# Kernel tuning notes

Hardware: AMD Instinct MI355X
Metric: run time of the kernel (lower is better)

Reference implementation:

```python
import jax, jax.numpy as jnp
import numpy as np

N, E, G, H, NI, EI, OUT, L = 100000, 800000, 256, 96, 32, 10, 256, 3


def setup_inputs() -> dict:
    key = jax.random.key(0)
    ks = jax.random.split(key, 32)
    s = 0.05  # small weight scale to keep activations finite over 3 layers
    d = {}
    d['x'] = jax.random.normal(ks[0], (N, NI), dtype=jnp.float32)
    d['edge_attr'] = jax.random.normal(ks[1], (E, EI), dtype=jnp.float32)
    d['edge_index'] = jax.random.randint(ks[2], (2, E), 0, N)
    d['batch_idx'] = jnp.sort(jax.random.randint(ks[3], (N,), 0, G))
    d['node_W'] = jax.random.normal(ks[4], (NI, H)) * s
    d['node_b'] = jnp.zeros((H,))
    d['edge_W'] = jax.random.normal(ks[5], (EI, H)) * s
    d['edge_b'] = jnp.zeros((H,))
    d['mlp_W1'] = jax.random.normal(ks[6], (L, H, H)) * s
    d['mlp_b1'] = jnp.zeros((L, H))
    d['mlp_W2'] = jax.random.normal(ks[7], (L, H, H)) * s
    d['mlp_b2'] = jnp.zeros((L, H))
    d['eps'] = jnp.zeros((L,))            # GINEConv train_eps, init 0
    d['gn_w'] = jnp.ones((L, H))          # GraphNorm weight
    d['gn_b'] = jnp.zeros((L, H))         # GraphNorm bias
    d['gn_ms'] = jnp.ones((L, H))         # GraphNorm mean_scale
    d['ln_g'] = jnp.ones((2 * H,))        # LayerNorm gamma
    d['ln_b'] = jnp.zeros((2 * H,))       # LayerNorm beta
    d['out_W1'] = jax.random.normal(ks[8], (2 * H, H)) * s
    d['out_b1'] = jnp.zeros((H,))
    d['out_W2'] = jax.random.normal(ks[9], (H, OUT)) * s
    d['out_b2'] = jnp.zeros((OUT,))
    return d


def reference(x, edge_attr, edge_index, batch_idx, node_W, node_b, edge_W, edge_b,
              mlp_W1, mlp_b1, mlp_W2, mlp_b2, eps, gn_w, gn_b, gn_ms,
              ln_g, ln_b, out_W1, out_b1, out_W2, out_b2):
    n = x.shape[0]
    src, dst = edge_index[0], edge_index[1]
    h = jax.nn.relu(x @ node_W + node_b)            # [N, H]
    e = jax.nn.relu(edge_attr @ edge_W + edge_b)    # [E, H]
    cnt = jax.ops.segment_sum(jnp.ones((n, 1), h.dtype), batch_idx, num_segments=G)
    cnt = jnp.maximum(cnt, 1.0)
    for i in range(L):
        res = h
        # GINEConv: msg = relu(x_src + e), sum-aggregate at dst
        msg = jax.nn.relu(h[src] + e)
        agg = jax.ops.segment_sum(msg, dst, num_segments=n)
        z = (1.0 + eps[i]) * h + agg
        z = jax.nn.relu(z @ mlp_W1[i] + mlp_b1[i]) @ mlp_W2[i] + mlp_b2[i]
        # GraphNorm (per-graph, per-feature)
        mean = jax.ops.segment_sum(z, batch_idx, num_segments=G) / cnt
        out = z - mean[batch_idx] * gn_ms[i]
        var = jax.ops.segment_sum(out * out, batch_idx, num_segments=G) / cnt
        z = gn_w[i] * out / jnp.sqrt(var + 1e-5)[batch_idx] + gn_b[i]
        h = jax.nn.relu(z) + res  # dropout is identity in eval
    gmean = jax.ops.segment_sum(h, batch_idx, num_segments=G) / cnt
    gmax = jax.ops.segment_max(h, batch_idx, num_segments=G)
    g = jnp.concatenate([gmean, gmax], axis=1)       # [G, 2H]
    mu = g.mean(axis=-1, keepdims=True)
    va = jnp.mean((g - mu) ** 2, axis=-1, keepdims=True)
    g = (g - mu) / jnp.sqrt(va + 1e-5) * ln_g + ln_b
    return jax.nn.relu(g @ out_W1 + out_b1) @ out_W2 + out_b2
```

## Files before the change

### kernel.cpp

```cpp
#include <hip/hip_runtime.h>
#include <hip/hip_bf16.h>
#include <cfloat>

#define Nn 100000
#define Ee 800000
#define Gg 256
#define NBLK ((Nn + 255) / 256)

typedef __attribute__((ext_vector_type(8))) short short8;
typedef __attribute__((ext_vector_type(4))) float f32x4;
typedef unsigned short u16;

static __device__ __forceinline__ float blo(unsigned u) { return __builtin_bit_cast(float, u << 16); }
static __device__ __forceinline__ float bhi(unsigned u) { return __builtin_bit_cast(float, u & 0xffff0000u); }
static __device__ __forceinline__ float bus(u16 u) { return __builtin_bit_cast(float, ((unsigned)u) << 16); }
static __device__ __forceinline__ u16 f2bu(float f) {
  __hip_bfloat16 b = __float2bfloat16(f);
  return __builtin_bit_cast(u16, b);
}
static __device__ __forceinline__ unsigned pack2(float lo, float hi) {
  return (unsigned)f2bu(lo) | ((unsigned)f2bu(hi) << 16);
}


__global__ __launch_bounds__(512) void k_gptr(const int* __restrict__ batch, int* __restrict__ gptr) {
  int g = threadIdx.x;
  if (g > Gg) return;
  if (g == Gg) { gptr[Gg] = Nn; return; }
  int lo = 0, hi = Nn;
  while (lo < hi) { int mid = (lo + hi) >> 1; if (batch[mid] < g) lo = mid + 1; else hi = mid; }
  gptr[g] = lo;
}

__global__ __launch_bounds__(256) void k_deg(const int* __restrict__ dst, int* __restrict__ deg) {
  int e = blockIdx.x * 256 + threadIdx.x;
  if (e < Ee) atomicAdd(&deg[dst[e]], 1);
}

__global__ __launch_bounds__(256) void k_scanA(const int* __restrict__ deg, int* __restrict__ localA,
                                               int* __restrict__ bsum) {
  __shared__ int ts[256];
  int t = threadIdx.x, b = blockIdx.x;
  int base = b * 1024 + t * 4;
  int v[4]; int s = 0;
#pragma unroll
  for (int k = 0; k < 4; k++) { int idx = base + k; v[k] = (idx < Nn) ? deg[idx] : 0; s += v[k]; }
  ts[t] = s; __syncthreads();
  for (int off = 1; off < 256; off <<= 1) {
    int y = (t >= off) ? ts[t - off] : 0;
    __syncthreads();
    ts[t] += y;
    __syncthreads();
  }
  int ex = ts[t] - s;
#pragma unroll
  for (int k = 0; k < 4; k++) { int idx = base + k; if (idx < Nn) localA[idx] = ex; ex += v[k]; }
  if (t == 255) bsum[b] = ts[255];
}

__global__ __launch_bounds__(128) void k_scanB(int* __restrict__ bsum) {
  __shared__ int s[128];
  const int NB = (Nn + 1023) / 1024;
  int t = threadIdx.x;
  int v = (t < NB) ? bsum[t] : 0;
  s[t] = v; __syncthreads();
  for (int off = 1; off < 128; off <<= 1) {
    int y = (t >= off) ? s[t - off] : 0;
    __syncthreads();
    s[t] += y;
    __syncthreads();
  }
  if (t < NB) bsum[t] = s[t] - v;
}

__global__ __launch_bounds__(256) void k_scanC(const int* __restrict__ localA, const int* __restrict__ bsum,
                                               int* __restrict__ rowptr, int* __restrict__ cursor) {
  int i = blockIdx.x * 256 + threadIdx.x;
  if (i < Nn) { int v = localA[i] + bsum[i >> 10]; rowptr[i] = v; cursor[i] = v; }
  if (i == 0) rowptr[Nn] = Ee;
}

__global__ __launch_bounds__(256) void k_fill(const int* __restrict__ dst, int* __restrict__ cursor,
                                              int* __restrict__ elist) {
  int e = blockIdx.x * 256 + threadIdx.x;
  if (e < Ee) { int p = atomicAdd(&cursor[dst[e]], 1); elist[p] = e; }
}


__global__ __launch_bounds__(256) void k_dhistA(const int* __restrict__ deg, int* __restrict__ bhist) {
  __shared__ int lh[64];
  int t = threadIdx.x, blk = blockIdx.x;
  if (t < 64) lh[t] = 0;
  __syncthreads();
  int i = blk * 256 + t;
  if (i < Nn) atomicAdd(&lh[min(deg[i], 63)], 1);
  __syncthreads();
  if (t < 64) bhist[blk * 64 + t] = lh[t];
}

__global__ void k_dscanB(int* __restrict__ bhist, int* __restrict__ binbase) {
  int bin = threadIdx.x;
  int running = 0;
  for (int blk = 0; blk < NBLK; blk++) {
    int v = bhist[blk * 64 + bin];
    bhist[blk * 64 + bin] = running;
    running += v;
  }
  int tot = running;
  int x = tot;
#pragma unroll
  for (int off = 1; off < 64; off <<= 1) {
    int y = __shfl_up(x, off);
    if (bin >= off) x += y;
  }
  binbase[bin] = x - tot;
}

__global__ __launch_bounds__(256) void k_dfillC(const int* __restrict__ deg, const int* __restrict__ bhist,
                                                const int* __restrict__ binbase, int* __restrict__ nperm) {
  __shared__ int lh[64];
  int t = threadIdx.x, blk = blockIdx.x;
  if (t < 64) lh[t] = 0;
  __syncthreads();
  int i = blk * 256 + t;
  if (i < Nn) {
    int bin = min(deg[i], 63);
    int lrank = atomicAdd(&lh[bin], 1);
    nperm[binbase[bin] + bhist[blk * 64 + bin] + lrank] = i;
  }
}


#define EB 128

__global__ __launch_bounds__(192) void k_edge_mlp(const float* __restrict__ eattr, const int* __restrict__ elist,
                                                  const int* __restrict__ srcArr, const float* __restrict__ eW,
                                                  const float* __restrict__ eb, u16* __restrict__ ePerm,
                                                  int* __restrict__ srcPerm) {
  __shared__ float ea[EB][10];
  __shared__ float Ws[10 * 96];
  __shared__ float bs[96];
  int t = threadIdx.x;
  int q0 = blockIdx.x * EB;
  int m = min(EB, Ee - q0);
  for (int i = t; i < 960; i += 192) Ws[i] = eW[i];
  if (t < 96) bs[t] = eb[t];
  for (int i = t; i < m; i += 192) srcPerm[q0 + i] = srcArr[elist[q0 + i]];
  for (int i = t; i < 5 * m; i += 192) {
    int ii = i / 5, k2 = (i - ii * 5) * 2;
    int e = elist[q0 + ii];
    *reinterpret_cast<float2*>(&ea[ii][k2]) = *reinterpret_cast<const float2*>(&eattr[(size_t)e * 10 + k2]);
  }
  __syncthreads();
  int j = (t % 48) * 2, sub = t / 48;
  float b0 = bs[j], b1 = bs[j + 1];
  for (int i = sub; i < m; i += 4) {
    float acc0 = b0, acc1 = b1;
#pragma unroll
    for (int k = 0; k < 10; k++) {
      float a = ea[i][k];
      float2 w = *reinterpret_cast<const float2*>(&Ws[k * 96 + j]);
      acc0 += a * w.x; acc1 += a * w.y;
    }
    *reinterpret_cast<unsigned*>(ePerm + (size_t)(q0 + i) * 96 + j) =
        pack2(fmaxf(acc0, 0.f), fmaxf(acc1, 0.f));
  }
}


__global__ __launch_bounds__(256) void k_node_mlp(const float* __restrict__ x, const float* __restrict__ W,
                                                  const float* __restrict__ b, u16* __restrict__ h16) {
  __shared__ float xs[16][33];
  __shared__ float Ws[32 * 96];
  __shared__ float bs[96];
  int t = threadIdx.x;
  int n0 = blockIdx.x * 16;
  for (int i = t; i < 32 * 96; i += 256) Ws[i] = W[i];
  if (t < 96) bs[t] = b[t];
  for (int i = t; i < 512; i += 256) {
    int nl = i >> 5, k = i & 31; int n = n0 + nl;
    xs[nl][k] = (n < Nn) ? x[n * 32 + k] : 0.f;
  }
  __syncthreads();
#pragma unroll
  for (int p = 0; p < 6; p++) {
    int oi = t + p * 256; int nl = oi / 96, j = oi % 96; int n = n0 + nl;
    if (n < Nn) {
      float acc = bs[j];
#pragma unroll
      for (int k = 0; k < 32; k++) acc += xs[nl][k] * Ws[k * 96 + j];
      h16[(size_t)n * 96 + j] = f2bu(fmaxf(acc, 0.f));
    }
  }
}


#define MPAD 104

#define ACC8(hv, ev, B) \
  acc[B+0] += fmaxf(blo(hv.x) + blo(ev.x), 0.f); acc[B+1] += fmaxf(bhi(hv.x) + bhi(ev.x), 0.f); \
  acc[B+2] += fmaxf(blo(hv.y) + blo(ev.y), 0.f); acc[B+3] += fmaxf(bhi(hv.y) + bhi(ev.y), 0.f); \
  acc[B+4] += fmaxf(blo(hv.z) + blo(ev.z), 0.f); acc[B+5] += fmaxf(bhi(hv.z) + bhi(ev.z), 0.f); \
  acc[B+6] += fmaxf(blo(hv.w) + blo(ev.w), 0.f); acc[B+7] += fmaxf(bhi(hv.w) + bhi(ev.w), 0.f);

#define LOAD6(hp, ep, H0, H1, H2, E0, E1, E2) \
  uint4 H0 = *reinterpret_cast<const uint4*>(hp); \
  uint4 H1 = *reinterpret_cast<const uint4*>(hp + 8); \
  uint4 H2 = *reinterpret_cast<const uint4*>(hp + 16); \
  uint4 E0 = *reinterpret_cast<const uint4*>(ep); \
  uint4 E1 = *reinterpret_cast<const uint4*>(ep + 8); \
  uint4 E2 = *reinterpret_cast<const uint4*>(ep + 16);

__global__ __launch_bounds__(256) void k_layer(const u16* __restrict__ h16,
                                               const u16* __restrict__ ePerm,
                                               const int* __restrict__ srcPerm,
                                               const int* __restrict__ rowptr,
                                               const int* __restrict__ nperm,
                                               const float* __restrict__ W1, const float* __restrict__ b1,
                                               const float* __restrict__ W2, const float* __restrict__ b2,
                                               const float* __restrict__ epsA, int layer,
                                               float* __restrict__ z) {
  __shared__ __align__(16) __hip_bfloat16 At[64][MPAD];
  __shared__ __align__(16) __hip_bfloat16 Wt[96][MPAD];
  __shared__ int snode[64], sbeg[64], send[64];
  int t = threadIdx.x;
  int n0 = blockIdx.x * 64;
  if (t < 64) {
    int idx = n0 + t;
    int node = (idx < Nn) ? nperm[idx] : -1;
    snode[t] = node;
    sbeg[t] = (node >= 0) ? rowptr[node] : 0;
    send[t] = (node >= 0) ? rowptr[node + 1] : 0;
  }
  __syncthreads();
  float epsv = 1.0f + epsA[layer];
  int nl = t >> 2, q = t & 3;
  int beg = sbeg[nl], end = send[nl];
  int node = snode[nl];
  const size_t fo = (size_t)q * 24;
  float acc[24];
#pragma unroll
  for (int j = 0; j < 24; j++) acc[j] = 0.f;
  int e = beg;
  for (; e + 3 <= end; e += 3) {
    int s0 = srcPerm[e], s1 = srcPerm[e + 1], s2 = srcPerm[e + 2];
    const u16* hp0 = h16 + (size_t)s0 * 96 + fo;
    const u16* hp1 = h16 + (size_t)s1 * 96 + fo;
    const u16* hp2 = h16 + (size_t)s2 * 96 + fo;
    const u16* ep0 = ePerm + (size_t)e * 96 + fo;
    const u16* ep1 = ePerm + (size_t)(e + 1) * 96 + fo;
    const u16* ep2 = ePerm + (size_t)(e + 2) * 96 + fo;
    LOAD6(hp0, ep0, ha0, ha1, ha2, ea0, ea1, ea2)
    LOAD6(hp1, ep1, hb0, hb1, hb2, eb0, eb1, eb2)
    LOAD6(hp2, ep2, hc0, hc1, hc2, ec0, ec1, ec2)
    ACC8(ha0, ea0, 0)
    ACC8(ha1, ea1, 8)
    ACC8(ha2, ea2, 16)
    ACC8(hb0, eb0, 0)
    ACC8(hb1, eb1, 8)
    ACC8(hb2, eb2, 16)
    ACC8(hc0, ec0, 0)
    ACC8(hc1, ec1, 8)
    ACC8(hc2, ec2, 16)
  }
  for (; e < end; e++) {
    int s0 = srcPerm[e];
    const u16* hp0 = h16 + (size_t)s0 * 96 + fo;
    const u16* ep0 = ePerm + (size_t)e * 96 + fo;
    LOAD6(hp0, ep0, ha0, ha1, ha2, ea0, ea1, ea2)
    ACC8(ha0, ea0, 0)
    ACC8(ha1, ea1, 8)
    ACC8(ha2, ea2, 16)
  }
  {
    uint4 hh0 = make_uint4(0, 0, 0, 0), hh1 = hh0, hh2 = hh0;
    if (node >= 0) {
      const u16* hp = h16 + (size_t)node * 96 + fo;
      hh0 = *reinterpret_cast<const uint4*>(hp);
      hh1 = *reinterpret_cast<const uint4*>(hp + 8);
      hh2 = *reinterpret_cast<const uint4*>(hp + 16);
    }
    uint4 w0, w1, w2;
    w0.x = pack2(fmaf(epsv, blo(hh0.x), acc[0]),  fmaf(epsv, bhi(hh0.x), acc[1]));
    w0.y = pack2(fmaf(epsv, blo(hh0.y), acc[2]),  fmaf(epsv, bhi(hh0.y), acc[3]));
    w0.z = pack2(fmaf(epsv, blo(hh0.z), acc[4]),  fmaf(epsv, bhi(hh0.z), acc[5]));
    w0.w = pack2(fmaf(epsv, blo(hh0.w), acc[6]),  fmaf(epsv, bhi(hh0.w), acc[7]));
    w1.x = pack2(fmaf(epsv, blo(hh1.x), acc[8]),  fmaf(epsv, bhi(hh1.x), acc[9]));
    w1.y = pack2(fmaf(epsv, blo(hh1.y), acc[10]), fmaf(epsv, bhi(hh1.y), acc[11]));
    w1.z = pack2(fmaf(epsv, blo(hh1.z), acc[12]), fmaf(epsv, bhi(hh1.z), acc[13]));
    w1.w = pack2(fmaf(epsv, blo(hh1.w), acc[14]), fmaf(epsv, bhi(hh1.w), acc[15]));
    w2.x = pack2(fmaf(epsv, blo(hh2.x), acc[16]), fmaf(epsv, bhi(hh2.x), acc[17]));
    w2.y = pack2(fmaf(epsv, blo(hh2.y), acc[18]), fmaf(epsv, bhi(hh2.y), acc[19]));
    w2.z = pack2(fmaf(epsv, blo(hh2.z), acc[20]), fmaf(epsv, bhi(hh2.z), acc[21]));
    w2.w = pack2(fmaf(epsv, blo(hh2.w), acc[22]), fmaf(epsv, bhi(hh2.w), acc[23]));
    *reinterpret_cast<uint4*>(&At[nl][fo]) = w0;
    *reinterpret_cast<uint4*>(&At[nl][fo + 8]) = w1;
    *reinterpret_cast<uint4*>(&At[nl][fo + 16]) = w2;
  }
  for (int i = t; i < 24 * 96; i += 256) {
    int kg = i / 96, c = i - kg * 96;
    int k0 = kg * 4;
    float w0 = W1[(k0 + 0) * 96 + c];
    float w1 = W1[(k0 + 1) * 96 + c];
    float w2 = W1[(k0 + 2) * 96 + c];
    float w3 = W1[(k0 + 3) * 96 + c];
    *reinterpret_cast<uint2*>(&Wt[c][k0]) = make_uint2(pack2(w0, w1), pack2(w2, w3));
  }
  __syncthreads();
  int w = t >> 6, l = t & 63;
  int lr = l & 15, lg = l >> 4;
  int rowBase = w * 16;
  short8 a0 = *reinterpret_cast<const short8*>(&At[rowBase + lr][lg * 8]);
  short8 a1 = *reinterpret_cast<const short8*>(&At[rowBase + lr][32 + lg * 8]);
  short8 a2 = *reinterpret_cast<const short8*>(&At[rowBase + lr][64 + lg * 8]);
  f32x4 gacc[6];
#pragma unroll
  for (int nt = 0; nt < 6; nt++) gacc[nt] = (f32x4){0.f, 0.f, 0.f, 0.f};
#pragma unroll
  for (int nt = 0; nt < 6; nt++) {
    short8 b0 = *reinterpret_cast<const short8*>(&Wt[nt * 16 + lr][lg * 8]);
    short8 bv1 = *reinterpret_cast<const short8*>(&Wt[nt * 16 + lr][32 + lg * 8]);
    short8 bv2 = *reinterpret_cast<const short8*>(&Wt[nt * 16 + lr][64 + lg * 8]);
    gacc[nt] = __builtin_amdgcn_mfma_f32_16x16x32_bf16(a0, b0, gacc[nt], 0, 0, 0);
    gacc[nt] = __builtin_amdgcn_mfma_f32_16x16x32_bf16(a1, bv1, gacc[nt], 0, 0, 0);
    gacc[nt] = __builtin_amdgcn_mfma_f32_16x16x32_bf16(a2, bv2, gacc[nt], 0, 0, 0);
  }
#pragma unroll
  for (int nt = 0; nt < 6; nt++) {
    int col = nt * 16 + lr;
    float bias = b1[col];
#pragma unroll
    for (int j = 0; j < 4; j++) {
      int row = rowBase + lg * 4 + j;
      At[row][col] = __float2bfloat16(fmaxf(gacc[nt][j] + bias, 0.f));
    }
  }
  __syncthreads();
  for (int i = t; i < 24 * 96; i += 256) {
    int kg = i / 96, c = i - kg * 96;
    int k0 = kg * 4;
    float w0 = W2[(k0 + 0) * 96 + c];
    float w1 = W2[(k0 + 1) * 96 + c];
    float w2 = W2[(k0 + 2) * 96 + c];
    float w3 = W2[(k0 + 3) * 96 + c];
    *reinterpret_cast<uint2*>(&Wt[c][k0]) = make_uint2(pack2(w0, w1), pack2(w2, w3));
  }
  __syncthreads();
  short8 m0 = *reinterpret_cast<const short8*>(&At[rowBase + lr][lg * 8]);
  short8 m1 = *reinterpret_cast<const short8*>(&At[rowBase + lr][32 + lg * 8]);
  short8 m2 = *reinterpret_cast<const short8*>(&At[rowBase + lr][64 + lg * 8]);
#pragma unroll
  for (int nt = 0; nt < 6; nt++) gacc[nt] = (f32x4){0.f, 0.f, 0.f, 0.f};
#pragma unroll
  for (int nt = 0; nt < 6; nt++) {
    short8 b0 = *reinterpret_cast<const short8*>(&Wt[nt * 16 + lr][lg * 8]);
    short8 bv1 = *reinterpret_cast<const short8*>(&Wt[nt * 16 + lr][32 + lg * 8]);
    short8 bv2 = *reinterpret_cast<const short8*>(&Wt[nt * 16 + lr][64 + lg * 8]);
    gacc[nt] = __builtin_amdgcn_mfma_f32_16x16x32_bf16(m0, b0, gacc[nt], 0, 0, 0);
    gacc[nt] = __builtin_amdgcn_mfma_f32_16x16x32_bf16(m1, bv1, gacc[nt], 0, 0, 0);
    gacc[nt] = __builtin_amdgcn_mfma_f32_16x16x32_bf16(m2, bv2, gacc[nt], 0, 0, 0);
  }
#pragma unroll
  for (int nt = 0; nt < 6; nt++) {
    int col = nt * 16 + lr;
    float bias = b2[col];
#pragma unroll
    for (int j = 0; j < 4; j++) {
      int row = rowBase + lg * 4 + j;
      int n = snode[row];
      if (n >= 0) z[(size_t)n * 96 + col] = gacc[nt][j] + bias;
    }
  }
}


#define ACHUNK 32

__global__ __launch_bounds__(128) void k_agg(const u16* __restrict__ h16, const float* __restrict__ eattr,
                                             const int* __restrict__ srcArr, const int* __restrict__ rowptr,
                                             const int* __restrict__ elist, const float* __restrict__ eW,
                                             const float* __restrict__ eb, float* __restrict__ agg) {
  __shared__ float Ws[10 * 96];
  __shared__ float bs_s[96];
  __shared__ int sL[ACHUNK];
  __shared__ float eaL[ACHUNK][10];
  int t = threadIdx.x;
  int nd = blockIdx.x;
  for (int i = t; i < 960; i += 128) Ws[i] = eW[i];
  if (t < 96) bs_s[t] = eb[t];
  int beg = rowptr[nd], end = rowptr[nd + 1];
  float acc = 0.f;
  for (int cs = beg; cs < end; cs += ACHUNK) {
    int m = min(ACHUNK, end - cs);
    __syncthreads();
    if (t < m) sL[t] = srcArr[elist[cs + t]];
    for (int i = t; i < 10 * m; i += 128) {
      int ii = i / 10, k = i - ii * 10;
      int e = elist[cs + ii];
      eaL[ii][k] = eattr[(size_t)e * 10 + k];
    }
    __syncthreads();
    if (t < 96) {
#pragma unroll 4
      for (int i = 0; i < m; i++) {
        int src = sL[i];
        float ej = bs_s[t];
#pragma unroll
        for (int k = 0; k < 10; k++) ej += eaL[i][k] * Ws[k * 96 + t];
        ej = fmaxf(ej, 0.f);
        acc += fmaxf(bus(h16[(size_t)src * 96 + t]) + ej, 0.f);
      }
    }
  }
  if (t < 96) agg[(size_t)nd * 96 + t] = acc;
}


__global__ __launch_bounds__(256) void k_mlp_fb(const u16* __restrict__ h16, const float* agg,
                                                const float* __restrict__ W1, const float* __restrict__ b1,
                                                const float* __restrict__ W2, const float* __restrict__ b2,
                                                const float* __restrict__ epsA, int layer, float* z) {
  __shared__ __align__(16) __hip_bfloat16 At[64][MPAD];
  __shared__ __align__(16) __hip_bfloat16 Wt[96][MPAD];
  __shared__ __align__(16) __hip_bfloat16 md[64][MPAD];
  int t = threadIdx.x;
  int n0 = blockIdx.x * 64;
  float epsv = 1.0f + epsA[layer];
  for (int i = t; i < 64 * 24; i += 256) {
    int r = i / 24, sl = (i - r * 24) * 4;
    int n = n0 + r;
    unsigned plo = 0, phi = 0;
    if (n < Nn) {
      uint2 hv = *reinterpret_cast<const uint2*>(h16 + (size_t)n * 96 + sl);
      float4 av = *reinterpret_cast<const float4*>(agg + (size_t)n * 96 + sl);
      plo = pack2(epsv * blo(hv.x) + av.x, epsv * bhi(hv.x) + av.y);
      phi = pack2(epsv * blo(hv.y) + av.z, epsv * bhi(hv.y) + av.w);
    }
    *reinterpret_cast<uint2*>(&At[r][sl]) = make_uint2(plo, phi);
  }
  for (int i = t; i < 24 * 96; i += 256) {
    int kg = i / 96, c = i - kg * 96;
    int k0 = kg * 4;
    float w0 = W1[(k0 + 0) * 96 + c];
    float w1 = W1[(k0 + 1) * 96 + c];
    float w2 = W1[(k0 + 2) * 96 + c];
    float w3 = W1[(k0 + 3) * 96 + c];
    *reinterpret_cast<uint2*>(&Wt[c][k0]) = make_uint2(pack2(w0, w1), pack2(w2, w3));
  }
  __syncthreads();
  int w = t >> 6, l = t & 63;
  int lr = l & 15, lg = l >> 4;
  int rowBase = w * 16;
  short8 a0 = *reinterpret_cast<const short8*>(&At[rowBase + lr][lg * 8]);
  short8 a1 = *reinterpret_cast<const short8*>(&At[rowBase + lr][32 + lg * 8]);
  short8 a2 = *reinterpret_cast<const short8*>(&At[rowBase + lr][64 + lg * 8]);
  f32x4 acc[6];
#pragma unroll
  for (int nt = 0; nt < 6; nt++) acc[nt] = (f32x4){0.f, 0.f, 0.f, 0.f};
#pragma unroll
  for (int nt = 0; nt < 6; nt++) {
    short8 b0 = *reinterpret_cast<const short8*>(&Wt[nt * 16 + lr][lg * 8]);
    short8 bv1 = *reinterpret_cast<const short8*>(&Wt[nt * 16 + lr][32 + lg * 8]);
    short8 bv2 = *reinterpret_cast<const short8*>(&Wt[nt * 16 + lr][64 + lg * 8]);
    acc[nt] = __builtin_amdgcn_mfma_f32_16x16x32_bf16(a0, b0, acc[nt], 0, 0, 0);
    acc[nt] = __builtin_amdgcn_mfma_f32_16x16x32_bf16(a1, bv1, acc[nt], 0, 0, 0);
    acc[nt] = __builtin_amdgcn_mfma_f32_16x16x32_bf16(a2, bv2, acc[nt], 0, 0, 0);
  }
#pragma unroll
  for (int nt = 0; nt < 6; nt++) {
    int col = nt * 16 + lr;
    float bias = b1[col];
#pragma unroll
    for (int j = 0; j < 4; j++) {
      int row = rowBase + lg * 4 + j;
      md[row][col] = __float2bfloat16(fmaxf(acc[nt][j] + bias, 0.f));
    }
  }
  __syncthreads();
  for (int i = t; i < 24 * 96; i += 256) {
    int kg = i / 96, c = i - kg * 96;
    int k0 = kg * 4;
    float w0 = W2[(k0 + 0) * 96 + c];
    float w1 = W2[(k0 + 1) * 96 + c];
    float w2 = W2[(k0 + 2) * 96 + c];
    float w3 = W2[(k0 + 3) * 96 + c];
    *reinterpret_cast<uint2*>(&Wt[c][k0]) = make_uint2(pack2(w0, w1), pack2(w2, w3));
  }
  __syncthreads();
  short8 m0 = *reinterpret_cast<const short8*>(&md[rowBase + lr][lg * 8]);
  short8 m1 = *reinterpret_cast<const short8*>(&md[rowBase + lr][32 + lg * 8]);
  short8 m2 = *reinterpret_cast<const short8*>(&md[rowBase + lr][64 + lg * 8]);
#pragma unroll
  for (int nt = 0; nt < 6; nt++) acc[nt] = (f32x4){0.f, 0.f, 0.f, 0.f};
#pragma unroll
  for (int nt = 0; nt < 6; nt++) {
    short8 b0 = *reinterpret_cast<const short8*>(&Wt[nt * 16 + lr][lg * 8]);
    short8 bv1 = *reinterpret_cast<const short8*>(&Wt[nt * 16 + lr][32 + lg * 8]);
    short8 bv2 = *reinterpret_cast<const short8*>(&Wt[nt * 16 + lr][64 + lg * 8]);
    acc[nt] = __builtin_amdgcn_mfma_f32_16x16x32_bf16(m0, b0, acc[nt], 0, 0, 0);
    acc[nt] = __builtin_amdgcn_mfma_f32_16x16x32_bf16(m1, bv1, acc[nt], 0, 0, 0);
    acc[nt] = __builtin_amdgcn_mfma_f32_16x16x32_bf16(m2, bv2, acc[nt], 0, 0, 0);
  }
#pragma unroll
  for (int nt = 0; nt < 6; nt++) {
    int col = nt * 16 + lr;
    float bias = b2[col];
#pragma unroll
    for (int j = 0; j < 4; j++) {
      int row = rowBase + lg * 4 + j;
      int n = n0 + row;
      if (n < Nn) z[(size_t)n * 96 + col] = acc[nt][j] + bias;
    }
  }
}


__global__ __launch_bounds__(384) void k_gnorm(const float* __restrict__ z, u16* __restrict__ h16,
                                               const int* __restrict__ gptr, const float* __restrict__ ms,
                                               const float* __restrict__ gw, const float* __restrict__ gb) {
  __shared__ float r1[16][100];
  __shared__ float r2[16][100];
  __shared__ float smm[96], sinv[96], sgb[96];
  int g = blockIdx.x, t = threadIdx.x;
  int beg = gptr[g], end = gptr[g + 1];
  int sub = t / 24, slot = t - (t / 24) * 24;
  int sl = slot * 4;
  float4 s1 = make_float4(0.f, 0.f, 0.f, 0.f), s2 = s1;
  for (int n = beg + sub; n < end; n += 16) {
    float4 zv = *reinterpret_cast<const float4*>(z + (size_t)n * 96 + sl);
    s1.x += zv.x; s1.y += zv.y; s1.z += zv.z; s1.w += zv.w;
    s2.x += zv.x * zv.x; s2.y += zv.y * zv.y; s2.z += zv.z * zv.z; s2.w += zv.w * zv.w;
  }
  *reinterpret_cast<float4*>(&r1[sub][sl]) = s1;
  *reinterpret_cast<float4*>(&r2[sub][sl]) = s2;
  __syncthreads();
  if (t < 96) {
    float S1 = 0.f, S2 = 0.f;
#pragma unroll
    for (int u = 0; u < 16; u++) { S1 += r1[u][t]; S2 += r2[u][t]; }
    float c = (float)max(end - beg, 1);
    float m = S1 / c;
    float mm = m * ms[t];
    float var = S2 / c - 2.f * mm * m + mm * mm;
    var = fmaxf(var, 0.f);
    smm[t] = mm;
    sinv[t] = rsqrtf(var + 1e-5f) * gw[t];
    sgb[t] = gb[t];
  }
  __syncthreads();
  float4 mm4 = *reinterpret_cast<const float4*>(&smm[sl]);
  float4 iv4 = *reinterpret_cast<const float4*>(&sinv[sl]);
  float4 gb4 = *reinterpret_cast<const float4*>(&sgb[sl]);
  for (int n = beg + sub; n < end; n += 16) {
    float4 zv = *reinterpret_cast<const float4*>(z + (size_t)n * 96 + sl);
    uint2 hv = *reinterpret_cast<const uint2*>(h16 + (size_t)n * 96 + sl);
    float o0 = fmaxf((zv.x - mm4.x) * iv4.x + gb4.x, 0.f) + blo(hv.x);
    float o1 = fmaxf((zv.y - mm4.y) * iv4.y + gb4.y, 0.f) + bhi(hv.x);
    float o2 = fmaxf((zv.z - mm4.z) * iv4.z + gb4.z, 0.f) + blo(hv.y);
    float o3 = fmaxf((zv.w - mm4.w) * iv4.w + gb4.w, 0.f) + bhi(hv.y);
    *reinterpret_cast<uint2*>(h16 + (size_t)n * 96 + sl) = make_uint2(pack2(o0, o1), pack2(o2, o3));
  }
}


__global__ __launch_bounds__(256) void k_pool_out(const u16* __restrict__ h16, const int* __restrict__ gptr,
                                                  const float* __restrict__ lng, const float* __restrict__ lnb,
                                                  const float* __restrict__ W1, const float* __restrict__ b1,
                                                  const float* __restrict__ W2, const float* __restrict__ b2,
                                                  float* __restrict__ out) {
  __shared__ float sh1[2][96], sh2[2][96];
  __shared__ float gbuf[192];
  __shared__ float rs[4], rq[4];
  __shared__ float s_mu, s_rstd;
  __shared__ float inter[96];
  int g = blockIdx.x, t = threadIdx.x;
  int beg = gptr[g], end = gptr[g + 1];
  if (t < 192) {
    int j = t % 96, half = t / 96;
    float s = 0.f, m = -INFINITY;
    for (int n = beg + half; n < end; n += 2) {
      float v = bus(h16[(size_t)n * 96 + j]);
      s += v; m = fmaxf(m, v);
    }
    sh1[half][j] = s; sh2[half][j] = m;
  }
  __syncthreads();
  if (t < 96) {
    float c = (float)max(end - beg, 1);
    gbuf[t] = (sh1[0][t] + sh1[1][t]) / c;
    gbuf[96 + t] = fmaxf(sh2[0][t], sh2[1][t]);
  }
  __syncthreads();
  float sv = (t < 192) ? gbuf[t] : 0.f;
  float qv = sv * sv;
#pragma unroll
  for (int off = 32; off; off >>= 1) { sv += __shfl_down(sv, off); qv += __shfl_down(qv, off); }
  if ((t & 63) == 0) { rs[t >> 6] = sv; rq[t >> 6] = qv; }
  __syncthreads();
  if (t == 0) {
    float S = rs[0] + rs[1] + rs[2] + rs[3];
    float Q = rq[0] + rq[1] + rq[2] + rq[3];
    float mu = S / 192.f;
    float va = Q / 192.f - mu * mu;
    s_mu = mu; s_rstd = rsqrtf(fmaxf(va, 0.f) + 1e-5f);
  }
  __syncthreads();
  if (t < 192) gbuf[t] = (gbuf[t] - s_mu) * s_rstd * lng[t] + lnb[t];
  __syncthreads();
  if (t < 96) {
    float a = b1[t];
    for (int k = 0; k < 192; k++) a += gbuf[k] * W1[k * 96 + t];
    inter[t] = fmaxf(a, 0.f);
  }
  __syncthreads();
  {
    float a = b2[t];
    for (int j = 0; j < 96; j++) a += inter[j] * W2[j * 256 + t];
    out[g * 256 + t] = a;
  }
}


extern "C" void kernel_launch(void* const* d_in, const int* in_sizes, int n_in,
                              void* d_out, int out_size, void* d_ws, size_t ws_size,
                              hipStream_t stream) {
  (void)in_sizes; (void)n_in; (void)out_size;
  const float* x     = (const float*)d_in[0];
  const float* eattr = (const float*)d_in[1];
  const int*   eidx2 = (const int*)  d_in[2];
  const int*   batch = (const int*)  d_in[3];
  const float* nodeW = (const float*)d_in[4];
  const float* nodeb = (const float*)d_in[5];
  const float* edgeW = (const float*)d_in[6];
  const float* edgeb = (const float*)d_in[7];
  const float* mlpW1 = (const float*)d_in[8];
  const float* mlpb1 = (const float*)d_in[9];
  const float* mlpW2 = (const float*)d_in[10];
  const float* mlpb2 = (const float*)d_in[11];
  const float* epsA  = (const float*)d_in[12];
  const float* gnw   = (const float*)d_in[13];
  const float* gnb   = (const float*)d_in[14];
  const float* gnms  = (const float*)d_in[15];
  const float* lng   = (const float*)d_in[16];
  const float* lnb   = (const float*)d_in[17];
  const float* oW1   = (const float*)d_in[18];
  const float* ob1   = (const float*)d_in[19];
  const float* oW2   = (const float*)d_in[20];
  const float* ob2   = (const float*)d_in[21];
  float* out = (float*)d_out;

  const int* srcArr = eidx2;
  const int* dstArr = eidx2 + Ee;

  char* p = (char*)d_ws;
  auto carve = [&](size_t bytes) -> void* {
    void* r = (void*)p;
    p += ((bytes + 255) & ~(size_t)255);
    return r;
  };
  u16* h16     = (u16*)carve((size_t)Nn * 96 * 2);
  float* aggz  = (float*)carve((size_t)Nn * 96 * 4);
  int* rowptr  = (int*)carve((size_t)(Nn + 1) * 4);
  int* elist   = (int*)carve((size_t)Ee * 4);
  int* gptr    = (int*)carve((size_t)(Gg + 1) * 4);
  int* nperm   = (int*)carve((size_t)Nn * 4);
  int* bhist   = (int*)carve((size_t)NBLK * 64 * 4);
  int* binbase = (int*)carve(64 * 4);
  int* srcPerm = (int*)carve((size_t)Ee * 4);
  int* deg     = srcPerm;
  int* localA  = srcPerm + Nn;
  int* cursor  = srcPerm + 2 * Nn;
  int* bsum    = srcPerm + 3 * Nn;
  u16* ePerm = (u16*)carve((size_t)Ee * 96 * 2);
  bool pre = ((size_t)(p - (char*)d_ws)) <= ws_size;

  hipMemsetAsync(deg, 0, (size_t)Nn * 4, stream);
  k_gptr<<<1, 512, 0, stream>>>(batch, gptr);
  k_deg<<<(Ee + 255) / 256, 256, 0, stream>>>(dstArr, deg);
  k_scanA<<<(Nn + 1023) / 1024, 256, 0, stream>>>(deg, localA, bsum);
  k_scanB<<<1, 128, 0, stream>>>(bsum);
  k_scanC<<<(Nn + 255) / 256, 256, 0, stream>>>(localA, bsum, rowptr, cursor);
  k_fill<<<(Ee + 255) / 256, 256, 0, stream>>>(dstArr, cursor, elist);

  if (pre) {
    k_dhistA<<<NBLK, 256, 0, stream>>>(deg, bhist);
    k_dscanB<<<1, 64, 0, stream>>>(bhist, binbase);
    k_dfillC<<<NBLK, 256, 0, stream>>>(deg, bhist, binbase, nperm);
    k_edge_mlp<<<(Ee + EB - 1) / EB, 192, 0, stream>>>(eattr, elist, srcArr, edgeW, edgeb, ePerm, srcPerm);
  }

  k_node_mlp<<<(Nn + 15) / 16, 256, 0, stream>>>(x, nodeW, nodeb, h16);

  for (int i = 0; i < 3; i++) {
    if (pre) {
      k_layer<<<(Nn + 63) / 64, 256, 0, stream>>>(h16, ePerm, srcPerm, rowptr, nperm,
                                                  mlpW1 + i * 9216, mlpb1 + i * 96,
                                                  mlpW2 + i * 9216, mlpb2 + i * 96, epsA, i, aggz);
    } else {
      k_agg<<<Nn, 128, 0, stream>>>(h16, eattr, srcArr, rowptr, elist, edgeW, edgeb, aggz);
      k_mlp_fb<<<(Nn + 63) / 64, 256, 0, stream>>>(h16, aggz, mlpW1 + i * 9216, mlpb1 + i * 96,
                                                   mlpW2 + i * 9216, mlpb2 + i * 96, epsA, i, aggz);
    }
    k_gnorm<<<Gg, 384, 0, stream>>>(aggz, h16, gptr, gnms + i * 96, gnw + i * 96, gnb + i * 96);
  }

  k_pool_out<<<Gg, 256, 0, stream>>>(h16, gptr, lng, lnb, oW1, ob1, oW2, ob2, out);
}
```

Measured before the change: 591.4 us.

## Build CSR in degree-sorted node order so layer edges are contiguous per block

The CSR row pointers and the edge list are now built in the degree-sorted node permutation order. A rank array maps each original node to its sorted position, and the scan and fill run over that order. Each layer block's edges then form one contiguous range, so the ePerm and srcPerm reads are sequential across the block and rowptr loads become a single coalesced 65-entry read. The cost is an extra rank kernel and indirect gathers in the scan and fill, and the fallback path keeps the original CSR.

```diff
diff --git a/kernel.cpp b/kernel.cpp
--- a/kernel.cpp
+++ b/kernel.cpp
@@ -45,6 +45,27 @@
   int v[4]; int s = 0;
 #pragma unroll
   for (int k = 0; k < 4; k++) { int idx = base + k; v[k] = (idx < Nn) ? deg[idx] : 0; s += v[k]; }
+  ts[t] = s; __syncthreads();
+  for (int off = 1; off < 256; off <<= 1) {
+    int y = (t >= off) ? ts[t - off] : 0;
+    __syncthreads();
+    ts[t] += y;
+    __syncthreads();
+  }
+  int ex = ts[t] - s;
+#pragma unroll
+  for (int k = 0; k < 4; k++) { int idx = base + k; if (idx < Nn) localA[idx] = ex; ex += v[k]; }
+  if (t == 255) bsum[b] = ts[255];
+}
+
+__global__ __launch_bounds__(256) void k_scanA2(const int* __restrict__ deg, const int* __restrict__ nperm,
+                                                int* __restrict__ localA, int* __restrict__ bsum) {
+  __shared__ int ts[256];
+  int t = threadIdx.x, b = blockIdx.x;
+  int base = b * 1024 + t * 4;
+  int v[4]; int s = 0;
+#pragma unroll
+  for (int k = 0; k < 4; k++) { int idx = base + k; v[k] = (idx < Nn) ? deg[nperm[idx]] : 0; s += v[k]; }
   ts[t] = s; __syncthreads();
   for (int off = 1; off < 256; off <<= 1) {
     int y = (t >= off) ? ts[t - off] : 0;
@@ -86,6 +107,12 @@
   if (e < Ee) { int p = atomicAdd(&cursor[dst[e]], 1); elist[p] = e; }
 }
 
+__global__ __launch_bounds__(256) void k_fill2(const int* __restrict__ dst, const int* __restrict__ rank,
+                                               int* __restrict__ cursor, int* __restrict__ elist) {
+  int e = blockIdx.x * 256 + threadIdx.x;
+  if (e < Ee) { int p = atomicAdd(&cursor[rank[dst[e]]], 1); elist[p] = e; }
+}
+
 
 __global__ __launch_bounds__(256) void k_dhistA(const int* __restrict__ deg, int* __restrict__ bhist) {
   __shared__ int lh[64];
@@ -128,6 +155,11 @@
     int lrank = atomicAdd(&lh[bin], 1);
     nperm[binbase[bin] + bhist[blk * 64 + bin] + lrank] = i;
   }
+}
+
+__global__ __launch_bounds__(256) void k_rank(const int* __restrict__ nperm, int* __restrict__ rank) {
+  int i = blockIdx.x * 256 + threadIdx.x;
+  if (i < Nn) rank[nperm[i]] = i;
 }
 
 
@@ -222,20 +254,16 @@
                                                float* __restrict__ z) {
   __shared__ __align__(16) __hip_bfloat16 At[64][MPAD];
   __shared__ __align__(16) __hip_bfloat16 Wt[96][MPAD];
-  __shared__ int snode[64], sbeg[64], send[64];
+  __shared__ int rp[65];
+  __shared__ int snode[64];
   int t = threadIdx.x;
   int n0 = blockIdx.x * 64;
-  if (t < 64) {
-    int idx = n0 + t;
-    int node = (idx < Nn) ? nperm[idx] : -1;
-    snode[t] = node;
-    sbeg[t] = (node >= 0) ? rowptr[node] : 0;
-    send[t] = (node >= 0) ? rowptr[node + 1] : 0;
-  }
+  if (t < 65) rp[t] = rowptr[min(n0 + t, Nn)];
+  if (t < 64) snode[t] = (n0 + t < Nn) ? nperm[n0 + t] : -1;
   __syncthreads();
   float epsv = 1.0f + epsA[layer];
   int nl = t >> 2, q = t & 3;
-  int beg = sbeg[nl], end = send[nl];
+  int beg = rp[nl], end = rp[nl + 1];
   int node = snode[nl];
   const size_t fo = (size_t)q * 24;
   float acc[24];
@@ -664,6 +692,7 @@
   int* elist   = (int*)carve((size_t)Ee * 4);
   int* gptr    = (int*)carve((size_t)(Gg + 1) * 4);
   int* nperm   = (int*)carve((size_t)Nn * 4);
+  int* rank    = (int*)carve((size_t)Nn * 4);
   int* bhist   = (int*)carve((size_t)NBLK * 64 * 4);
   int* binbase = (int*)carve(64 * 4);
   int* srcPerm = (int*)carve((size_t)Ee * 4);
@@ -677,16 +706,22 @@
   hipMemsetAsync(deg, 0, (size_t)Nn * 4, stream);
   k_gptr<<<1, 512, 0, stream>>>(batch, gptr);
   k_deg<<<(Ee + 255) / 256, 256, 0, stream>>>(dstArr, deg);
-  k_scanA<<<(Nn + 1023) / 1024, 256, 0, stream>>>(deg, localA, bsum);
-  k_scanB<<<1, 128, 0, stream>>>(bsum);
-  k_scanC<<<(Nn + 255) / 256, 256, 0, stream>>>(localA, bsum, rowptr, cursor);
-  k_fill<<<(Ee + 255) / 256, 256, 0, stream>>>(dstArr, cursor, elist);
 
   if (pre) {
     k_dhistA<<<NBLK, 256, 0, stream>>>(deg, bhist);
     k_dscanB<<<1, 64, 0, stream>>>(bhist, binbase);
     k_dfillC<<<NBLK, 256, 0, stream>>>(deg, bhist, binbase, nperm);
+    k_rank<<<NBLK, 256, 0, stream>>>(nperm, rank);
+    k_scanA2<<<(Nn + 1023) / 1024, 256, 0, stream>>>(deg, nperm, localA, bsum);
+    k_scanB<<<1, 128, 0, stream>>>(bsum);
+    k_scanC<<<(Nn + 255) / 256, 256, 0, stream>>>(localA, bsum, rowptr, cursor);
+    k_fill2<<<(Ee + 255) / 256, 256, 0, stream>>>(dstArr, rank, cursor, elist);
     k_edge_mlp<<<(Ee + EB - 1) / EB, 192, 0, stream>>>(eattr, elist, srcArr, edgeW, edgeb, ePerm, srcPerm);
+  } else {
+    k_scanA<<<(Nn + 1023) / 1024, 256, 0, stream>>>(deg, localA, bsum);
+    k_scanB<<<1, 128, 0, stream>>>(bsum);
+    k_scanC<<<(Nn + 255) / 256, 256, 0, stream>>>(localA, bsum, rowptr, cursor);
+    k_fill<<<(Ee + 255) / 256, 256, 0, stream>>>(dstArr, cursor, elist);
   }
 
   k_node_mlp<<<(Nn + 15) / 16, 256, 0, stream>>>(x, nodeW, nodeb, h16);
```

Result: no change. 582.4 us (-1.5%).
